# Kernel optimization log

Measured on AMD Instinct MI355X. Metric: run time of the kernel, lower is better.

Reference implementation:

```python
import jax, jax.numpy as jnp
import numpy as np

N = 50000      # num_nodes
E = 600000     # num_edges
DIN = 3
D = 128        # hidden_dim == output_dim
H = 4          # heads
C = D // H     # per-head channels = 32
L = 3          # num_layers
NEG_SLOPE = 0.2
LN_EPS = 1e-5


def setup_inputs() -> dict:
    key = jax.random.key(0)
    ks = jax.random.split(key, 14)
    s = 1.0 / np.sqrt(D)
    return {
        "x": jax.random.normal(ks[0], (E, DIN), dtype=jnp.float32),
        "edge_index": jax.random.randint(ks[1], (2, E), 0, N, dtype=jnp.int32),
        "W_edge": jax.random.normal(ks[2], (DIN, D), dtype=jnp.float32) / np.sqrt(DIN),
        "b_edge": jnp.zeros((D,), jnp.float32),
        "W_node": jax.random.normal(ks[3], (D, D), dtype=jnp.float32) * s,
        "b_node": jnp.zeros((D,), jnp.float32),
        "lin_w": jax.random.normal(ks[4], (L, D, D), dtype=jnp.float32) * s,   # GATConv lin (bias=False)
        "att_src": jax.random.normal(ks[5], (L, H, C), dtype=jnp.float32) * s,
        "att_dst": jax.random.normal(ks[6], (L, H, C), dtype=jnp.float32) * s,
        "gat_bias": jnp.zeros((L, D), jnp.float32),
        "ln_g": jnp.ones((L, D), jnp.float32),
        "ln_b": jnp.zeros((L, D), jnp.float32),
        "num_nodes": N,
    }


def _layernorm(x, g, b):
    mu = x.mean(-1, keepdims=True)
    var = ((x - mu) ** 2).mean(-1, keepdims=True)
    return (x - mu) * jax.lax.rsqrt(var + LN_EPS) * g + b


def reference(x, edge_index, W_edge, b_edge, W_node, b_node,
              lin_w, att_src, att_dst, gat_bias, ln_g, ln_b, num_nodes):
    n = num_nodes
    row, col = edge_index[0], edge_index[1]

    # Edge -> node scatter-mean init (x has edge features, E != N)
    edge_h = x @ W_edge + b_edge                                   # [E, D]
    h = jax.ops.segment_sum(edge_h, col, num_segments=n)           # [N, D]
    cnt = jax.ops.segment_sum(jnp.ones((E,), x.dtype), col, num_segments=n)
    h = h / jnp.clip(cnt, 1.0)[:, None]
    h = h @ W_node + b_node

    # self-loops (PyG GATConv default add_self_loops=True)
    loop = jnp.arange(n, dtype=row.dtype)
    src = jnp.concatenate([row, loop])                             # [E+N]
    dst = jnp.concatenate([col, loop])

    for i in range(L):
        xh = (h @ lin_w[i]).reshape(n, H, C)                       # [N, H, C]
        a_s = (xh * att_src[i]).sum(-1)                            # [N, H]
        a_d = (xh * att_dst[i]).sum(-1)
        e = jax.nn.leaky_relu(a_s[src] + a_d[dst], NEG_SLOPE)      # [E+N, H]
        # segment softmax over incoming edges per destination node
        m = jax.ops.segment_max(e, dst, num_segments=n)            # [N, H]
        ex = jnp.exp(e - m[dst])
        denom = jax.ops.segment_sum(ex, dst, num_segments=n)       # [N, H]
        alpha = ex / denom[dst]                                    # [E+N, H]
        out = jax.ops.segment_sum(alpha[:, :, None] * xh[src], dst,
                                  num_segments=n)                  # [N, H, C]
        h_new = out.reshape(n, D) + gat_bias[i]
        h_new = _layernorm(h_new, ln_g[i], ln_b[i])
        if i < L - 1:
            h_new = jax.nn.relu(h_new)
        h = h + h_new                                              # residual (dims match)
    return h
```

## Files before the change

### kernel.cpp

```cpp
#include <hip/hip_runtime.h>
#include <hip/hip_bf16.h>
#include <math.h>

#define D 128
#define H 4
#define NEG_SLOPE 0.2f
#define LN_EPS 1e-5f
#define LDA 136
#define LDE 132

using bf16x8 = __attribute__((ext_vector_type(8))) short;
using f32x4  = __attribute__((ext_vector_type(4))) float;

__device__ __forceinline__ float lrelu(float v) {
    return v > 0.f ? v : NEG_SLOPE * v;
}
__device__ __forceinline__ unsigned short bfb(float f) {
    __hip_bfloat16 h = __float2bfloat16(f);
    return *reinterpret_cast<unsigned short*>(&h);
}

__global__ void k_rank(const int* __restrict__ ei, int* __restrict__ cnt,
                       int* __restrict__ rank, int E) {
    int e = blockIdx.x * blockDim.x + threadIdx.x;
    if (e >= E) return;
    rank[e] = atomicAdd(&cnt[ei[E + e]], 1);
}

__global__ void k_scan_part(const int* __restrict__ cnt, int* __restrict__ off,
                            int* __restrict__ bsum, int N) {
    __shared__ int sm[256];
    int i = blockIdx.x * 256 + threadIdx.x;
    int v = (i < N) ? cnt[i] : 0;
    sm[threadIdx.x] = v;
    __syncthreads();
    #pragma unroll
    for (int o = 1; o < 256; o <<= 1) {
        int t = (threadIdx.x >= (unsigned)o) ? sm[threadIdx.x - o] : 0;
        __syncthreads();
        sm[threadIdx.x] += t;
        __syncthreads();
    }
    if (i < N) off[i] = sm[threadIdx.x];
    if (threadIdx.x == 255) bsum[blockIdx.x] = sm[255];
}

__global__ void k_scan_top(int* __restrict__ bsum, int* __restrict__ off,
                           int NB, int N) {
    __shared__ int sm[256];
    int v = (threadIdx.x < (unsigned)NB) ? bsum[threadIdx.x] : 0;
    sm[threadIdx.x] = v;
    __syncthreads();
    #pragma unroll
    for (int o = 1; o < 256; o <<= 1) {
        int t = (threadIdx.x >= (unsigned)o) ? sm[threadIdx.x - o] : 0;
        __syncthreads();
        sm[threadIdx.x] += t;
        __syncthreads();
    }
    if (threadIdx.x < (unsigned)NB) bsum[threadIdx.x] = sm[threadIdx.x] - v;
    if (threadIdx.x == 255) off[N] = sm[255];
}

__global__ void k_scan_add(const int* __restrict__ cnt, int* __restrict__ off,
                           const int* __restrict__ bsum, int N) {
    int i = blockIdx.x * 256 + threadIdx.x;
    if (i < N) off[i] = off[i] - cnt[i] + bsum[blockIdx.x];
}

__global__ void k_fill(const int* __restrict__ ei, const int* __restrict__ off,
                       const int* __restrict__ rank, int2* __restrict__ adj2, int E) {
    int e = blockIdx.x * blockDim.x + threadIdx.x;
    if (e >= E) return;
    int dst = ei[E + e];
    int slot = off[dst] + rank[e];
    adj2[slot] = make_int2(ei[e], e);
}

__global__ __launch_bounds__(256) void k_wprep(
        const float* __restrict__ Wn, const float* __restrict__ lw,
        unsigned short* __restrict__ Wt) {
    __shared__ float Wf[32][132];
    int b = blockIdx.x, w = b >> 2, p = b & 3;
    const float* src = (w == 0) ? (Wn + (size_t)p * 32 * D)
                                : (lw + (size_t)(w - 1) * D * D + (size_t)p * 32 * D);
    int tid = threadIdx.x;
    #pragma unroll
    for (int j = 0; j < 4; j++) {
        int i = tid + j * 256;
        int r = i >> 5, q = i & 31;
        float4 v = reinterpret_cast<const float4*>(src)[i];
        *reinterpret_cast<float4*>(&Wf[r][q * 4]) = v;
    }
    __syncthreads();
    int n = tid & 127, ks = (tid >> 7) * 16;
    unsigned short t16[16];
    #pragma unroll
    for (int j = 0; j < 16; j++) t16[j] = bfb(Wf[ks + j][n]);
    unsigned short* dst = Wt + ((size_t)w * D + n) * D + p * 32 + ks;
    *reinterpret_cast<uint4*>(dst) = *reinterpret_cast<uint4*>(t16);
    *reinterpret_cast<uint4*>(dst + 8) = *reinterpret_cast<uint4*>(t16 + 8);
}

template <int MODE>
__global__ __launch_bounds__(512) void k_gemm(
        const float* __restrict__ A, const unsigned short* __restrict__ Wt,
        const float* __restrict__ bias, float* __restrict__ C,
        __hip_bfloat16* __restrict__ xhb, float* __restrict__ a_s,
        float* __restrict__ a_d, const float* __restrict__ att_s,
        const float* __restrict__ att_d,
        const float* __restrict__ x, const int2* __restrict__ adj2,
        const int* __restrict__ off,
        const float* __restrict__ W_edge, const float* __restrict__ b_edge,
        int N) {
    __shared__ __align__(16) unsigned short AsB[64 * LDA];
    __shared__ __align__(16) unsigned short WtB[128 * LDA];
    int tid = threadIdx.x;
    int n0 = blockIdx.x * 64;

    #pragma unroll
    for (int j = 0; j < 4; j++) {
        int ch = tid + j * 512;
        int r = ch >> 4, c = ch & 15;
        uint4 v = *reinterpret_cast<const uint4*>(Wt + (size_t)r * D + c * 8);
        *reinterpret_cast<uint4*>(&WtB[r * LDA + c * 8]) = v;
    }

    if (MODE == 2) {
        __shared__ float rowf[64][4];
        {
            int r = tid >> 3, t8v = tid & 7;
            int n = n0 + r;
            float s0 = 0.f, s1 = 0.f, s2 = 0.f;
            int degv = 0;
            if (n < N) {
                int beg = off[n], end = off[n + 1];
                degv = end - beg;
                for (int p = beg + t8v; p < end; p += 8) {
                    const float* xr = x + (size_t)adj2[p].y * 3;
                    s0 += xr[0]; s1 += xr[1]; s2 += xr[2];
                }
            }
            #pragma unroll
            for (int o = 1; o < 8; o <<= 1) {
                s0 += __shfl_xor(s0, o);
                s1 += __shfl_xor(s1, o);
                s2 += __shfl_xor(s2, o);
            }
            if (t8v == 0)
                *reinterpret_cast<float4*>(rowf[r]) =
                    make_float4(s0, s1, s2, (float)degv);
        }
        __syncthreads();
        #pragma unroll
        for (int j = 0; j < 2; j++) {
            int ch = tid + j * 512;
            int r = ch >> 4, c = ch & 15;
            float4 rv = *reinterpret_cast<float4*>(rowf[r]);
            float cn = rv.w, rc = 1.f / fmaxf(cn, 1.f);
            int d0 = c * 8;
            unsigned short t8[8];
            #pragma unroll
            for (int q = 0; q < 2; q++) {
                float4 we0 = *reinterpret_cast<const float4*>(W_edge + d0 + q * 4);
                float4 we1 = *reinterpret_cast<const float4*>(W_edge + D + d0 + q * 4);
                float4 we2 = *reinterpret_cast<const float4*>(W_edge + 2 * D + d0 + q * 4);
                float4 be  = *reinterpret_cast<const float4*>(b_edge + d0 + q * 4);
                t8[q * 4 + 0] = bfb((rv.x * we0.x + rv.y * we1.x + rv.z * we2.x + cn * be.x) * rc);
                t8[q * 4 + 1] = bfb((rv.x * we0.y + rv.y * we1.y + rv.z * we2.y + cn * be.y) * rc);
                t8[q * 4 + 2] = bfb((rv.x * we0.z + rv.y * we1.z + rv.z * we2.z + cn * be.z) * rc);
                t8[q * 4 + 3] = bfb((rv.x * we0.w + rv.y * we1.w + rv.z * we2.w + cn * be.w) * rc);
            }
            *reinterpret_cast<uint4*>(&AsB[r * LDA + c * 8]) =
                *reinterpret_cast<uint4*>(t8);
        }
    } else {
        #pragma unroll
        for (int j = 0; j < 2; j++) {
            int ch = tid + j * 512;
            int r = ch >> 4, c = ch & 15;
            int n = n0 + r;
            float4 v0 = make_float4(0.f, 0.f, 0.f, 0.f), v1 = v0;
            if (n < N) {
                v0 = reinterpret_cast<const float4*>(A)[(size_t)n * 32 + c * 2];
                v1 = reinterpret_cast<const float4*>(A)[(size_t)n * 32 + c * 2 + 1];
            }
            unsigned short t8[8] = {bfb(v0.x), bfb(v0.y), bfb(v0.z), bfb(v0.w),
                                    bfb(v1.x), bfb(v1.y), bfb(v1.z), bfb(v1.w)};
            *reinterpret_cast<uint4*>(&AsB[r * LDA + c * 8]) =
                *reinterpret_cast<uint4*>(t8);
        }
    }
    __syncthreads();

    int lane = tid & 63, wv = tid >> 6;
    int wr = wv & 3, wc = wv >> 2;
    int lrow = lane & 15, lk = lane >> 4;
    f32x4 acc[4];
    #pragma unroll
    for (int ct = 0; ct < 4; ct++) acc[ct] = (f32x4){0.f, 0.f, 0.f, 0.f};
    int arow = wr * 16 + lrow;
    #pragma unroll
    for (int ks = 0; ks < 4; ks++) {
        bf16x8 af = *reinterpret_cast<const bf16x8*>(
            &AsB[arow * LDA + ks * 32 + lk * 8]);
        #pragma unroll
        for (int ct = 0; ct < 4; ct++) {
            bf16x8 bfr = *reinterpret_cast<const bf16x8*>(
                &WtB[((wc * 4 + ct) * 16 + lrow) * LDA + ks * 32 + lk * 8]);
            acc[ct] = __builtin_amdgcn_mfma_f32_16x16x32_bf16(af, bfr, acc[ct], 0, 0, 0);
        }
    }
    __syncthreads();

    float* Ef = reinterpret_cast<float*>(WtB);
    #pragma unroll
    for (int ct = 0; ct < 4; ct++)
        #pragma unroll
        for (int j = 0; j < 4; j++)
            Ef[(wr * 16 + lk * 4 + j) * LDE + (wc * 4 + ct) * 16 + lrow] = acc[ct][j];
    __syncthreads();

    int tx = tid & 15, ty = tid >> 4;
    int c0 = tx * 8, r0 = ty * 2;
    float o[2][8];
    #pragma unroll
    for (int r = 0; r < 2; r++) {
        float4 v0 = *reinterpret_cast<const float4*>(&Ef[(r0 + r) * LDE + c0]);
        float4 v1 = *reinterpret_cast<const float4*>(&Ef[(r0 + r) * LDE + c0 + 4]);
        o[r][0] = v0.x; o[r][1] = v0.y; o[r][2] = v0.z; o[r][3] = v0.w;
        o[r][4] = v1.x; o[r][5] = v1.y; o[r][6] = v1.z; o[r][7] = v1.w;
    }

    if (MODE == 2) {
        float b[8];
        #pragma unroll
        for (int c = 0; c < 8; c++) b[c] = bias[c0 + c];
        #pragma unroll
        for (int r = 0; r < 2; r++) {
            int n = n0 + r0 + r;
            if (n >= N) continue;
            float4 o0 = make_float4(o[r][0] + b[0], o[r][1] + b[1],
                                    o[r][2] + b[2], o[r][3] + b[3]);
            float4 o1 = make_float4(o[r][4] + b[4], o[r][5] + b[5],
                                    o[r][6] + b[6], o[r][7] + b[7]);
            reinterpret_cast<float4*>(C)[(size_t)n * 32 + tx * 2] = o0;
            reinterpret_cast<float4*>(C)[(size_t)n * 32 + tx * 2 + 1] = o1;
        }
    } else {
        float ats[8], atd[8];
        #pragma unroll
        for (int c = 0; c < 8; c++) { ats[c] = att_s[c0 + c]; atd[c] = att_d[c0 + c]; }
        #pragma unroll
        for (int r = 0; r < 2; r++) {
            int n = n0 + r0 + r;
            union { uint4 v; unsigned short s[8]; } pk;
            #pragma unroll
            for (int c = 0; c < 8; c++) pk.s[c] = bfb(o[r][c]);
            float ps = 0.f, pd = 0.f;
            #pragma unroll
            for (int c = 0; c < 8; c++) { ps += o[r][c] * ats[c]; pd += o[r][c] * atd[c]; }
            ps += __shfl_xor(ps, 1); ps += __shfl_xor(ps, 2);
            pd += __shfl_xor(pd, 1); pd += __shfl_xor(pd, 2);
            if (n < N) {
                *reinterpret_cast<uint4*>(xhb + (size_t)n * D + c0) = pk.v;
                if ((tx & 3) == 0) {
                    a_s[n * H + (tx >> 2)] = ps;
                    a_d[n * H + (tx >> 2)] = pd;
                }
            }
        }
    }
}

__global__ __launch_bounds__(256) void k_gat5(
        const __hip_bfloat16* __restrict__ xhb, const int* __restrict__ off,
        const int2* __restrict__ adj2, const float* __restrict__ a_s,
        const float* __restrict__ a_d, const float* __restrict__ bias,
        const float* __restrict__ g, const float* __restrict__ bln,
        float* __restrict__ h, int N, int do_relu) {
    int wid = threadIdx.x >> 6;
    int lane = threadIdx.x & 63;
    int n = blockIdx.x * 4 + wid;
    if (n >= N) return;

    int cl = lane & 15;
    int sub = lane >> 4;
    int hb = cl >> 2;
    int c0 = cl * 8;

    int beg = off[n], end = off[n + 1];
    int deg = end - beg;
    int items = deg + 1;
    int itp = (items + 3) & ~3;

    float adA = a_d[n * H + hb];
    float den = 0.f;
    float acc[8];
    #pragma unroll
    for (int c = 0; c < 8; c++) acc[c] = 0.f;

    #pragma unroll 4
    for (int pp = sub; pp < itp; pp += 4) {
        int s = (pp < deg) ? adj2[beg + pp].x : n;
        float av = a_s[(size_t)s * H + hb];
        uint4 u = *reinterpret_cast<const uint4*>(xhb + (size_t)s * D + c0);
        float e = lrelu(av + adA);
        float wv = (pp < items) ? __expf(e) : 0.f;
        den += wv;
        float f;
        f = __uint_as_float(u.x << 16);         acc[0] += wv * f;
        f = __uint_as_float(u.x & 0xffff0000u); acc[1] += wv * f;
        f = __uint_as_float(u.y << 16);         acc[2] += wv * f;
        f = __uint_as_float(u.y & 0xffff0000u); acc[3] += wv * f;
        f = __uint_as_float(u.z << 16);         acc[4] += wv * f;
        f = __uint_as_float(u.z & 0xffff0000u); acc[5] += wv * f;
        f = __uint_as_float(u.w << 16);         acc[6] += wv * f;
        f = __uint_as_float(u.w & 0xffff0000u); acc[7] += wv * f;
    }

    #pragma unroll
    for (int c = 0; c < 8; c++) {
        acc[c] += __shfl_xor(acc[c], 16);
        acc[c] += __shfl_xor(acc[c], 32);
    }
    den += __shfl_xor(den, 16);
    den += __shfl_xor(den, 32);
    float rden = 1.0f / den;

    float4 b0 = *reinterpret_cast<const float4*>(bias + c0);
    float4 b1 = *reinterpret_cast<const float4*>(bias + c0 + 4);
    float o[8];
    o[0] = acc[0] * rden + b0.x; o[1] = acc[1] * rden + b0.y;
    o[2] = acc[2] * rden + b0.z; o[3] = acc[3] * rden + b0.w;
    o[4] = acc[4] * rden + b1.x; o[5] = acc[5] * rden + b1.y;
    o[6] = acc[6] * rden + b1.z; o[7] = acc[7] * rden + b1.w;

    float s1 = 0.f;
    #pragma unroll
    for (int c = 0; c < 8; c++) s1 += o[c];
    #pragma unroll
    for (int os = 1; os < 64; os <<= 1) s1 += __shfl_xor(s1, os);
    float mu = s1 * (1.0f / 512.0f);
    float s2 = 0.f;
    #pragma unroll
    for (int c = 0; c < 8; c++) { float dv = o[c] - mu; s2 += dv * dv; }
    #pragma unroll
    for (int os = 1; os < 64; os <<= 1) s2 += __shfl_xor(s2, os);
    float inv = rsqrtf(s2 * (1.0f / 512.0f) + LN_EPS);

    if (sub == 0) {
        float4 g0 = *reinterpret_cast<const float4*>(g + c0);
        float4 g1 = *reinterpret_cast<const float4*>(g + c0 + 4);
        float4 l0 = *reinterpret_cast<const float4*>(bln + c0);
        float4 l1 = *reinterpret_cast<const float4*>(bln + c0 + 4);
        float y[8];
        y[0] = (o[0] - mu) * inv * g0.x + l0.x;
        y[1] = (o[1] - mu) * inv * g0.y + l0.y;
        y[2] = (o[2] - mu) * inv * g0.z + l0.z;
        y[3] = (o[3] - mu) * inv * g0.w + l0.w;
        y[4] = (o[4] - mu) * inv * g1.x + l1.x;
        y[5] = (o[5] - mu) * inv * g1.y + l1.y;
        y[6] = (o[6] - mu) * inv * g1.z + l1.z;
        y[7] = (o[7] - mu) * inv * g1.w + l1.w;
        if (do_relu) {
            #pragma unroll
            for (int c = 0; c < 8; c++) y[c] = fmaxf(y[c], 0.f);
        }
        float4 h0 = *reinterpret_cast<float4*>(h + (size_t)n * D + c0);
        float4 h1 = *reinterpret_cast<float4*>(h + (size_t)n * D + c0 + 4);
        h0.x += y[0]; h0.y += y[1]; h0.z += y[2]; h0.w += y[3];
        h1.x += y[4]; h1.y += y[5]; h1.z += y[6]; h1.w += y[7];
        *reinterpret_cast<float4*>(h + (size_t)n * D + c0) = h0;
        *reinterpret_cast<float4*>(h + (size_t)n * D + c0 + 4) = h1;
    }
}

extern "C" void kernel_launch(void* const* d_in, const int* in_sizes, int n_in,
                              void* d_out, int out_size, void* d_ws, size_t ws_size,
                              hipStream_t stream) {
    const float* x       = (const float*)d_in[0];
    const int*   ei      = (const int*)  d_in[1];
    const float* W_edge  = (const float*)d_in[2];
    const float* b_edge  = (const float*)d_in[3];
    const float* W_node  = (const float*)d_in[4];
    const float* b_node  = (const float*)d_in[5];
    const float* lin_w   = (const float*)d_in[6];
    const float* att_src = (const float*)d_in[7];
    const float* att_dst = (const float*)d_in[8];
    const float* gat_b   = (const float*)d_in[9];
    const float* ln_g    = (const float*)d_in[10];
    const float* ln_b    = (const float*)d_in[11];

    int N = out_size / D;
    int E = in_sizes[1] / 2;
    int NB = (N + 255) / 256;

    char* w = (char*)d_ws;
    auto carve = [&](size_t bytes) {
        void* p = (void*)w;
        w += (bytes + 255) & ~(size_t)255;
        return p;
    };
    int*   cnt  = (int*)  carve((size_t)N * 4);
    int*   off  = (int*)  carve((size_t)(N + 1) * 4);
    int*   rank = (int*)  carve((size_t)E * 4);
    int2*  adj2 = (int2*) carve((size_t)E * 8);
    int*   bsum = (int*)  carve((size_t)NB * 4);
    float* tmp  = (float*)carve((size_t)N * D * 4);
    float* a_s  = (float*)carve((size_t)N * H * 4);
    float* a_d  = (float*)carve((size_t)N * H * 4);
    unsigned short* Wt = (unsigned short*)carve((size_t)4 * D * D * 2);
    __hip_bfloat16* xhb = (__hip_bfloat16*)tmp;

    float* h = (float*)d_out;

    hipMemsetAsync(cnt, 0, (size_t)N * 4, stream);

    int tb = 256;
    k_wprep<<<16, 256, 0, stream>>>(W_node, lin_w, Wt);
    k_rank<<<(E + tb - 1) / tb, tb, 0, stream>>>(ei, cnt, rank, E);
    k_scan_part<<<NB, 256, 0, stream>>>(cnt, off, bsum, N);
    k_scan_top<<<1, 256, 0, stream>>>(bsum, off, NB, N);
    k_scan_add<<<NB, 256, 0, stream>>>(cnt, off, bsum, N);
    k_fill<<<(E + tb - 1) / tb, tb, 0, stream>>>(ei, off, rank, adj2, E);
    k_gemm<2><<<(N + 63) / 64, 512, 0, stream>>>(
        nullptr, Wt, b_node, h, nullptr, nullptr, nullptr, nullptr, nullptr,
        x, adj2, off, W_edge, b_edge, N);

    for (int i = 0; i < 3; i++) {
        k_gemm<1><<<(N + 63) / 64, 512, 0, stream>>>(
            h, Wt + (size_t)(i + 1) * D * D, nullptr, nullptr,
            xhb, a_s, a_d, att_src + i * D, att_dst + i * D,
            nullptr, nullptr, nullptr, nullptr, nullptr, N);
        k_gat5<<<(N + 3) / 4, 256, 0, stream>>>(
            xhb, off, adj2, a_s, a_d,
            gat_b + i * D, ln_g + i * D, ln_b + i * D,
            h, N, (i < 2) ? 1 : 0);
    }
}
```

Baseline: 231.5 us.

## Keep bf16 copy of h and pre-permute edge features into CSR order

The GAT and init kernels now also write a bf16 copy of h, so the per-layer GEMM loads half the bytes and skips the fp32-to-bf16 conversion. k_fill scatters the edge features x into CSR order, so the init gather reads them contiguously instead of going through edge ids. The adjacency shrinks from int2 to int. This adds extra bf16 writes and an E*3 float permuted copy in exchange for fewer and more coalesced reads.

```diff
diff --git a/kernel.cpp b/kernel.cpp
--- a/kernel.cpp
+++ b/kernel.cpp
@@ -69,12 +69,16 @@
 }
 
 __global__ void k_fill(const int* __restrict__ ei, const int* __restrict__ off,
-                       const int* __restrict__ rank, int2* __restrict__ adj2, int E) {
+                       const int* __restrict__ rank, const float* __restrict__ x,
+                       int* __restrict__ adj, float* __restrict__ xp, int E) {
     int e = blockIdx.x * blockDim.x + threadIdx.x;
     if (e >= E) return;
     int dst = ei[E + e];
     int slot = off[dst] + rank[e];
-    adj2[slot] = make_int2(ei[e], e);
+    adj[slot] = ei[e];
+    const float* xr = x + (size_t)e * 3;
+    float* d = xp + (size_t)slot * 3;
+    d[0] = xr[0]; d[1] = xr[1]; d[2] = xr[2];
 }
 
 __global__ __launch_bounds__(256) void k_wprep(
@@ -104,13 +108,14 @@
 
 template <int MODE>
 __global__ __launch_bounds__(512) void k_gemm(
-        const float* __restrict__ A, const unsigned short* __restrict__ Wt,
+        const unsigned short* __restrict__ hb_in,
+        const unsigned short* __restrict__ Wt,
         const float* __restrict__ bias, float* __restrict__ C,
+        unsigned short* __restrict__ hb_out,
         __hip_bfloat16* __restrict__ xhb, float* __restrict__ a_s,
         float* __restrict__ a_d, const float* __restrict__ att_s,
         const float* __restrict__ att_d,
-        const float* __restrict__ x, const int2* __restrict__ adj2,
-        const int* __restrict__ off,
+        const float* __restrict__ xp, const int* __restrict__ off,
         const float* __restrict__ W_edge, const float* __restrict__ b_edge,
         int N) {
     __shared__ __align__(16) unsigned short AsB[64 * LDA];
@@ -137,7 +142,7 @@
                 int beg = off[n], end = off[n + 1];
                 degv = end - beg;
                 for (int p = beg + t8v; p < end; p += 8) {
-                    const float* xr = x + (size_t)adj2[p].y * 3;
+                    const float* xr = xp + (size_t)p * 3;
                     s0 += xr[0]; s1 += xr[1]; s2 += xr[2];
                 }
             }
@@ -180,15 +185,10 @@
             int ch = tid + j * 512;
             int r = ch >> 4, c = ch & 15;
             int n = n0 + r;
-            float4 v0 = make_float4(0.f, 0.f, 0.f, 0.f), v1 = v0;
-            if (n < N) {
-                v0 = reinterpret_cast<const float4*>(A)[(size_t)n * 32 + c * 2];
-                v1 = reinterpret_cast<const float4*>(A)[(size_t)n * 32 + c * 2 + 1];
-            }
-            unsigned short t8[8] = {bfb(v0.x), bfb(v0.y), bfb(v0.z), bfb(v0.w),
-                                    bfb(v1.x), bfb(v1.y), bfb(v1.z), bfb(v1.w)};
-            *reinterpret_cast<uint4*>(&AsB[r * LDA + c * 8]) =
-                *reinterpret_cast<uint4*>(t8);
+            uint4 v = make_uint4(0, 0, 0, 0);
+            if (n < N)
+                v = *reinterpret_cast<const uint4*>(hb_in + (size_t)n * D + c * 8);
+            *reinterpret_cast<uint4*>(&AsB[r * LDA + c * 8]) = v;
         }
     }
     __syncthreads();
@@ -240,12 +240,17 @@
         for (int r = 0; r < 2; r++) {
             int n = n0 + r0 + r;
             if (n >= N) continue;
-            float4 o0 = make_float4(o[r][0] + b[0], o[r][1] + b[1],
-                                    o[r][2] + b[2], o[r][3] + b[3]);
-            float4 o1 = make_float4(o[r][4] + b[4], o[r][5] + b[5],
-                                    o[r][6] + b[6], o[r][7] + b[7]);
+            float oo[8];
+            #pragma unroll
+            for (int c = 0; c < 8; c++) oo[c] = o[r][c] + b[c];
+            float4 o0 = make_float4(oo[0], oo[1], oo[2], oo[3]);
+            float4 o1 = make_float4(oo[4], oo[5], oo[6], oo[7]);
             reinterpret_cast<float4*>(C)[(size_t)n * 32 + tx * 2] = o0;
             reinterpret_cast<float4*>(C)[(size_t)n * 32 + tx * 2 + 1] = o1;
+            union { uint4 v; unsigned short s[8]; } pk;
+            #pragma unroll
+            for (int c = 0; c < 8; c++) pk.s[c] = bfb(oo[c]);
+            *reinterpret_cast<uint4*>(hb_out + (size_t)n * D + c0) = pk.v;
         }
     } else {
         float ats[8], atd[8];
@@ -275,10 +280,11 @@
 
 __global__ __launch_bounds__(256) void k_gat5(
         const __hip_bfloat16* __restrict__ xhb, const int* __restrict__ off,
-        const int2* __restrict__ adj2, const float* __restrict__ a_s,
+        const int* __restrict__ adj, const float* __restrict__ a_s,
         const float* __restrict__ a_d, const float* __restrict__ bias,
         const float* __restrict__ g, const float* __restrict__ bln,
-        float* __restrict__ h, int N, int do_relu) {
+        float* __restrict__ h, unsigned short* __restrict__ hb,
+        int N, int do_relu) {
     int wid = threadIdx.x >> 6;
     int lane = threadIdx.x & 63;
     int n = blockIdx.x * 4 + wid;
@@ -286,7 +292,7 @@
 
     int cl = lane & 15;
     int sub = lane >> 4;
-    int hb = cl >> 2;
+    int hbd = cl >> 2;
     int c0 = cl * 8;
 
     int beg = off[n], end = off[n + 1];
@@ -294,7 +300,7 @@
     int items = deg + 1;
     int itp = (items + 3) & ~3;
 
-    float adA = a_d[n * H + hb];
+    float adA = a_d[n * H + hbd];
     float den = 0.f;
     float acc[8];
     #pragma unroll
@@ -302,8 +308,8 @@
 
     #pragma unroll 4
     for (int pp = sub; pp < itp; pp += 4) {
-        int s = (pp < deg) ? adj2[beg + pp].x : n;
-        float av = a_s[(size_t)s * H + hb];
+        int s = (pp < deg) ? adj[beg + pp] : n;
+        float av = a_s[(size_t)s * H + hbd];
         uint4 u = *reinterpret_cast<const uint4*>(xhb + (size_t)s * D + c0);
         float e = lrelu(av + adA);
         float wv = (pp < items) ? __expf(e) : 0.f;
@@ -373,6 +379,12 @@
         h1.x += y[4]; h1.y += y[5]; h1.z += y[6]; h1.w += y[7];
         *reinterpret_cast<float4*>(h + (size_t)n * D + c0) = h0;
         *reinterpret_cast<float4*>(h + (size_t)n * D + c0 + 4) = h1;
+        union { uint4 v; unsigned short s[8]; } pk;
+        pk.s[0] = bfb(h0.x); pk.s[1] = bfb(h0.y);
+        pk.s[2] = bfb(h0.z); pk.s[3] = bfb(h0.w);
+        pk.s[4] = bfb(h1.x); pk.s[5] = bfb(h1.y);
+        pk.s[6] = bfb(h1.z); pk.s[7] = bfb(h1.w);
+        *reinterpret_cast<uint4*>(hb + (size_t)n * D + c0) = pk.v;
     }
 }
 
@@ -405,13 +417,15 @@
     int*   cnt  = (int*)  carve((size_t)N * 4);
     int*   off  = (int*)  carve((size_t)(N + 1) * 4);
     int*   rank = (int*)  carve((size_t)E * 4);
-    int2*  adj2 = (int2*) carve((size_t)E * 8);
+    int*   adj  = (int*)  carve((size_t)E * 4);
+    float* xp   = (float*)carve((size_t)E * 3 * 4);
     int*   bsum = (int*)  carve((size_t)NB * 4);
     float* tmp  = (float*)carve((size_t)N * D * 4);
     float* a_s  = (float*)carve((size_t)N * H * 4);
     float* a_d  = (float*)carve((size_t)N * H * 4);
     unsigned short* Wt = (unsigned short*)carve((size_t)4 * D * D * 2);
     __hip_bfloat16* xhb = (__hip_bfloat16*)tmp;
+    unsigned short* hb  = (unsigned short*)((char*)tmp + (size_t)N * D * 2);
 
     float* h = (float*)d_out;
 
@@ -423,19 +437,19 @@
     k_scan_part<<<NB, 256, 0, stream>>>(cnt, off, bsum, N);
     k_scan_top<<<1, 256, 0, stream>>>(bsum, off, NB, N);
     k_scan_add<<<NB, 256, 0, stream>>>(cnt, off, bsum, N);
-    k_fill<<<(E + tb - 1) / tb, tb, 0, stream>>>(ei, off, rank, adj2, E);
+    k_fill<<<(E + tb - 1) / tb, tb, 0, stream>>>(ei, off, rank, x, adj, xp, E);
     k_gemm<2><<<(N + 63) / 64, 512, 0, stream>>>(
-        nullptr, Wt, b_node, h, nullptr, nullptr, nullptr, nullptr, nullptr,
-        x, adj2, off, W_edge, b_edge, N);
+        nullptr, Wt, b_node, h, hb, nullptr, nullptr, nullptr, nullptr, nullptr,
+        xp, off, W_edge, b_edge, N);
 
     for (int i = 0; i < 3; i++) {
         k_gemm<1><<<(N + 63) / 64, 512, 0, stream>>>(
-            h, Wt + (size_t)(i + 1) * D * D, nullptr, nullptr,
+            hb, Wt + (size_t)(i + 1) * D * D, nullptr, nullptr, nullptr,
             xhb, a_s, a_d, att_src + i * D, att_dst + i * D,
-            nullptr, nullptr, nullptr, nullptr, nullptr, N);
+            nullptr, nullptr, nullptr, nullptr, N);
         k_gat5<<<(N + 3) / 4, 256, 0, stream>>>(
-            xhb, off, adj2, a_s, a_d,
+            xhb, off, adj, a_s, a_d,
             gat_b + i * D, ln_g + i * D, ln_b + i * D,
-            h, N, (i < 2) ? 1 : 0);
-    }
-}
+            h, hb, N, (i < 2) ? 1 : 0);
+    }
+}
```

Measured after the change: 240.5 us. +3.9%, slower.
